# Optimization experiments

Measured on AMD Instinct MI355X. Metric: run time of the kernel, lower is better.

## Reference

```python
import jax, jax.numpy as jnp
import numpy as np

DIAG_PENALTY = 100.0

def setup_inputs() -> dict:
    key = jax.random.key(0)
    x = jax.random.normal(key, (8192, 768), dtype=jnp.float32)
    return {"x": x, "coef": 1.0, "tau": 1.0}

def _similarity(x):
    # sim[i, j] = -||x_i - x_j||^2, computed via GEMM expansion
    # ||a - b||^2 = ||a||^2 + ||b||^2 - 2 a.b  (avoids the (N,N,D) intermediate)
    sq = jnp.sum(x * x, axis=1)                      # [N]
    gram = x @ x.T                                   # [N, N]
    sim = 2.0 * gram - sq[:, None] - sq[None, :]     # = -||x_i - x_j||^2
    n = x.shape[0]
    sim = sim - DIAG_PENALTY * jnp.eye(n, dtype=x.dtype)
    return sim

def reference(x, coef, tau):
    sim = _similarity(x) * tau                       # [N, N]
    logp = jax.nn.log_softmax(sim, axis=-1)          # stable, single pass
    prob = jnp.exp(logp)
    entropy = -jnp.sum(prob * logp, axis=-1)         # [N]
    return coef * jnp.mean(entropy)
```

## Files before the change

### kernel.cpp

```cpp
#include <hip/hip_runtime.h>
#include <hip/hip_bf16.h>
#include <hip/hip_fp8.h>
#include <cstdint>
#include <cstddef>

#define GN 8192
#define GD 768
#define NB 64
#define NTILE 2080
#define KI 12

#define LOG2E 1.4426950408889634f
#define LN2 0.6931471805599453f

typedef __attribute__((ext_vector_type(4))) float f32x4;
typedef __attribute__((ext_vector_type(16))) float f32x16;
typedef __attribute__((ext_vector_type(4))) int i32x4;
typedef __attribute__((ext_vector_type(8))) int i32x8;

typedef __attribute__((address_space(1))) const unsigned int gu32;
typedef __attribute__((address_space(3))) unsigned int lu32;

#define SHUF8(L, H) __builtin_shufflevector(L, H, 0, 1, 2, 3, 4, 5, 6, 7)
#define Z16 {0.f, 0.f, 0.f, 0.f, 0.f, 0.f, 0.f, 0.f, 0.f, 0.f, 0.f, 0.f, 0.f, 0.f, 0.f, 0.f}
#define MXFMA(A, B, C) __builtin_amdgcn_mfma_scale_f32_32x32x64_f8f6f4( \
    A, B, C, 0, 0, 0, 0x7f7f7f7f, 0, 0x7f7f7f7f)

__device__ __forceinline__ void gl2lds16(const void* g, void* l) {
    __builtin_amdgcn_global_load_lds((gu32*)g, (lu32*)l, 16, 0, 0);
}

__device__ __forceinline__ float hexp2(float x) {
    return __builtin_amdgcn_exp2f(x);
}

template <int CTRL>
__device__ __forceinline__ float fdpp(float x) {
    return __int_as_float(__builtin_amdgcn_update_dpp(
        0, __float_as_int(x), CTRL, 0xF, 0xF, true));
}
__device__ __forceinline__ float qmax16(float v) {
    v = fmaxf(v, fdpp<0x128>(v));
    v = fmaxf(v, fdpp<0x124>(v));
    v = fmaxf(v, fdpp<0x122>(v));
    v = fmaxf(v, fdpp<0x121>(v));
    return v;
}
__device__ __forceinline__ float qsum16(float v) {
    v += fdpp<0x128>(v);
    v += fdpp<0x124>(v);
    v += fdpp<0x122>(v);
    v += fdpp<0x121>(v);
    return v;
}

__global__ __launch_bounds__(256) void prep_kernel(const float* __restrict__ x,
                                                   unsigned char* __restrict__ xq,
                                                   float* __restrict__ sq,
                                                   float* __restrict__ out) {
    if (blockIdx.x == 0 && threadIdx.x == 0) out[0] = 0.f;
    const int w = threadIdx.x >> 6, lane = threadIdx.x & 63;
    const int row = blockIdx.x * 4 + w;
    const float4* xr = (const float4*)(x + (size_t)row * GD);
    unsigned int* xqr = (unsigned int*)(xq + (size_t)row * GD);
    float s = 0.f;
#pragma unroll
    for (int i = 0; i < 3; ++i) {
        float4 v = xr[lane + 64 * i];
        unsigned int pk = __builtin_amdgcn_cvt_pk_fp8_f32(v.x, v.y, 0, false);
        pk = __builtin_amdgcn_cvt_pk_fp8_f32(v.z, v.w, pk, true);
        float d0 = __builtin_amdgcn_cvt_f32_fp8(pk, 0);
        float d1 = __builtin_amdgcn_cvt_f32_fp8(pk, 1);
        float d2 = __builtin_amdgcn_cvt_f32_fp8(pk, 2);
        float d3 = __builtin_amdgcn_cvt_f32_fp8(pk, 3);
        s += d0 * d0 + d1 * d1 + d2 * d2 + d3 * d3;
        xqr[lane + 64 * i] = pk;
    }
#pragma unroll
    for (int off = 1; off < 64; off <<= 1) s += __shfl_xor(s, off);
    if (lane == 0) sq[row] = s;
}

__global__ __launch_bounds__(256, 3) void sym_gemm_entropy(
    const unsigned char* __restrict__ xq, const float* __restrict__ sq,
    const float* __restrict__ taup, float* __restrict__ pm,
    float* __restrict__ ps, float* __restrict__ pt) {
    __shared__ __align__(16) char lds[16384];
    float (*tmrg)[4][3] = (float (*)[4][3])lds;

    const int tid = threadIdx.x;
    const int lane = tid & 63;
    const int w = tid >> 6;
    const int cl2 = lane & 31, hi = lane >> 5;

    const int b = blockIdx.x;
    int I = (int)((sqrtf(8.0f * (float)b + 1.0f) - 1.0f) * 0.5f);
    while ((I + 1) * (I + 2) / 2 <= b) ++I;
    while (I * (I + 1) / 2 > b) --I;
    const int J = b - I * (I + 1) / 2;
    const int row_base = I * 128;
    const int col_base = J * 128;
    const float taub = (*taup) * LOG2E;

    {
    }
    const int sS = tid & 127;
    const int ggS = tid >> 7;
    const int qloS = (sS >> 6) & 1, qhiS = (sS >> 5) & 1;
    const int r4S = (sS >> 4) & 1, r3S = (sS >> 3) & 1;
    const int rlowS = (sS & 7) ^ ((qhiS << 1) | r4S);
    const int rB = ggS * 32 + ((r4S << 4) | (r3S << 3) | rlowS);
    const int qB = (qhiS << 1) | qloS;
    const unsigned char* gB = xq + (size_t)(col_base + rB) * GD + qB * 16;

    const int r4L = (cl2 >> 4) & 1, r3L = (cl2 >> 3) & 1;
    const int bsl = (cl2 & 7) ^ ((hi << 1) | r4L);
    const int s0 = (hi << 5) | (r4L << 4) | (r3L << 3) | bsl;
    const int offB00 = 0 * 2048 + (s0 << 4), offB01 = offB00 + 1024;
    const int offB10 = 1 * 2048 + (s0 << 4), offB11 = offB10 + 1024;
    const int offB20 = 2 * 2048 + (s0 << 4), offB21 = offB20 + 1024;
    const int offB30 = 3 * 2048 + (s0 << 4), offB31 = offB30 + 1024;

    const unsigned char* gAr =
        xq + (size_t)(row_base + w * 32 + cl2) * GD + 32 * hi;

    f32x16 acc0 = Z16, acc1 = Z16, acc2 = Z16, acc3 = Z16;

    gl2lds16(gB, lds + tid * 16);
    gl2lds16(gB + (size_t)64 * GD, lds + 4096 + tid * 16);
    i32x4 aCL = *(const i32x4*)(gAr);
    i32x4 aCH = *(const i32x4*)(gAr + 16);
    i32x4 aNL = aCL, aNH = aCH;

#pragma unroll 2
    for (int kk = 0; kk < KI; ++kk) {
        __syncthreads();

        const char* Bb = lds + (kk & 1) * 8192;
        i32x4 b0L = *(const i32x4*)(Bb + offB00), b0H = *(const i32x4*)(Bb + offB01);
        i32x4 b1L = *(const i32x4*)(Bb + offB10), b1H = *(const i32x4*)(Bb + offB11);
        i32x4 b2L = *(const i32x4*)(Bb + offB20), b2H = *(const i32x4*)(Bb + offB21);
        i32x4 b3L = *(const i32x4*)(Bb + offB30), b3H = *(const i32x4*)(Bb + offB31);

        if (kk + 1 < KI) {
            char* Bn = lds + ((kk + 1) & 1) * 8192;
            const int ko = (kk + 1) * 64;
            gl2lds16(gB + ko, Bn + tid * 16);
            gl2lds16(gB + (size_t)64 * GD + ko, Bn + 4096 + tid * 16);
            aNL = *(const i32x4*)(gAr + ko);
            aNH = *(const i32x4*)(gAr + ko + 16);
        }

        i32x8 av = SHUF8(aCL, aCH);
        acc0 = MXFMA(av, SHUF8(b0L, b0H), acc0);
        acc1 = MXFMA(av, SHUF8(b1L, b1H), acc1);
        acc2 = MXFMA(av, SHUF8(b2L, b2H), acc2);
        acc3 = MXFMA(av, SHUF8(b3L, b3H), acc3);

        aCL = aNL;
        aCH = aNH;
    }

    f32x4 pa[4][4];
#define SPLIT16(TJ, A)                                          \
    pa[TJ][0] = __builtin_shufflevector(A, A, 0, 1, 2, 3);      \
    pa[TJ][1] = __builtin_shufflevector(A, A, 4, 5, 6, 7);      \
    pa[TJ][2] = __builtin_shufflevector(A, A, 8, 9, 10, 11);    \
    pa[TJ][3] = __builtin_shufflevector(A, A, 12, 13, 14, 15);
    SPLIT16(0, acc0)
    SPLIT16(1, acc1)
    SPLIT16(2, acc2)
    SPLIT16(3, acc3)
#undef SPLIT16

    const float t2 = 2.f * taub;
    const float pen = 100.f * taub;
    float ar[16];
#pragma unroll
    for (int q = 0; q < 4; ++q)
#pragma unroll
        for (int rg = 0; rg < 4; ++rg)
            ar[q * 4 + rg] = -taub * sq[row_base + w * 32 + rg + 8 * q + 4 * hi];
    float ac[4];
#pragma unroll
    for (int tj = 0; tj < 4; ++tj) ac[tj] = -taub * sq[col_base + tj * 32 + cl2];

    float* pmJ = pm + (size_t)J * GN;
    float* psJ = ps + (size_t)J * GN;
    float* ptJ = pt + (size_t)J * GN;

#pragma unroll
    for (int q = 0; q < 4; ++q)
#pragma unroll
        for (int rg = 0; rg < 4; ++rg) {
            const int rl = rg + 8 * q + 4 * hi;
            const int rglob = row_base + w * 32 + rl;
            float uu[4];
            float mloc = -1e30f;
            if (I == J) {
#pragma unroll
                for (int tj = 0; tj < 4; ++tj) {
                    float u = fmaf(t2, pa[tj][q][rg], ac[tj]);
                    if (rglob == col_base + tj * 32 + cl2) u -= pen;
                    uu[tj] = u;
                    mloc = fmaxf(mloc, u);
                }
            } else {
#pragma unroll
                for (int tj = 0; tj < 4; ++tj) {
                    float u = fmaf(t2, pa[tj][q][rg], ac[tj]);
                    uu[tj] = u;
                    mloc = fmaxf(mloc, u);
                }
            }
            mloc = fmaxf(mloc, __shfl_xor(mloc, 16));
            mloc = qmax16(mloc);
            float s = 0.f, t = 0.f;
#pragma unroll
            for (int tj = 0; tj < 4; ++tj) {
                float d = uu[tj] - mloc;
                float e = hexp2(d);
                s += e;
                t += e * d;
            }
            s += __shfl_xor(s, 16);
            t += __shfl_xor(t, 16);
            s = qsum16(s);
            t = qsum16(t);
            if (cl2 == 0) {
                pmJ[rglob] = mloc + ar[q * 4 + rg];
                psJ[rglob] = s;
                ptJ[rglob] = t;
            }
        }

    if (I != J) {
        __syncthreads();
#pragma unroll
        for (int tj = 0; tj < 4; ++tj) {
            float uu[16];
            float mloc = -1e30f;
#pragma unroll
            for (int q = 0; q < 4; ++q)
#pragma unroll
                for (int rg = 0; rg < 4; ++rg) {
                    float u = fmaf(t2, pa[tj][q][rg], ar[q * 4 + rg]);
                    uu[q * 4 + rg] = u;
                    mloc = fmaxf(mloc, u);
                }
            mloc = fmaxf(mloc, __shfl_xor(mloc, 32));
            float s = 0.f, t = 0.f;
#pragma unroll
            for (int k = 0; k < 16; ++k) {
                float d = uu[k] - mloc;
                float e = hexp2(d);
                s += e;
                t += e * d;
            }
            s += __shfl_xor(s, 32);
            t += __shfl_xor(t, 32);
            if (hi == 0) {
                int c = tj * 32 + cl2;
                tmrg[c][w][0] = mloc + ac[tj];
                tmrg[c][w][1] = s;
                tmrg[c][w][2] = t;
            }
        }
        __syncthreads();
        if (tid < 128) {
            float m = tmrg[tid][0][0], S = tmrg[tid][0][1], T = tmrg[tid][0][2];
#pragma unroll
            for (int ww = 1; ww < 4; ++ww) {
                float mc = tmrg[tid][ww][0], Sc = tmrg[tid][ww][1], Tc = tmrg[tid][ww][2];
                float mn = fmaxf(m, mc);
                float ea = hexp2(m - mn), eb = hexp2(mc - mn);
                T = (T + (m - mn) * S) * ea + (Tc + (mc - mn) * Sc) * eb;
                S = S * ea + Sc * eb;
                m = mn;
            }
            int c = col_base + tid;
            pm[(size_t)I * GN + c] = m;
            ps[(size_t)I * GN + c] = S;
            pt[(size_t)I * GN + c] = T;
        }
    }
}

__global__ __launch_bounds__(256) void combine(const float* __restrict__ pm,
                                               const float* __restrict__ ps,
                                               const float* __restrict__ pt,
                                               const float* __restrict__ coefp,
                                               float* __restrict__ out) {
    const int t = threadIdx.x;
    const int r = t & 63;
    const int chunk = t >> 6;
    const int row = blockIdx.x * 64 + r;
    float m = -1e30f, S = 0.f, T = 0.f;
#pragma unroll
    for (int i = 0; i < 16; ++i) {
        const int c = chunk * 16 + i;
        float mc = pm[(size_t)c * GN + row];
        float Sc = ps[(size_t)c * GN + row];
        float Tc = pt[(size_t)c * GN + row];
        float mn = fmaxf(m, mc);
        float ea = __builtin_amdgcn_exp2f(m - mn), eb = __builtin_amdgcn_exp2f(mc - mn);
        T = (T + (m - mn) * S) * ea + (Tc + (mc - mn) * Sc) * eb;
        S = S * ea + Sc * eb;
        m = mn;
    }
    __shared__ float lm[4][64], lS[4][64], lT[4][64];
    lm[chunk][r] = m;
    lS[chunk][r] = S;
    lT[chunk][r] = T;
    __syncthreads();
    if (t < 64) {
        float M = lm[0][r], Sa = lS[0][r], Ta = lT[0][r];
#pragma unroll
        for (int cc = 1; cc < 4; ++cc) {
            float mc = lm[cc][r], Sc = lS[cc][r], Tc = lT[cc][r];
            float mn = fmaxf(M, mc);
            float ea = __builtin_amdgcn_exp2f(M - mn), eb = __builtin_amdgcn_exp2f(mc - mn);
            Ta = (Ta + (M - mn) * Sa) * ea + (Tc + (mc - mn) * Sc) * eb;
            Sa = Sa * ea + Sc * eb;
            M = mn;
        }
        float ent2 = __log2f(Sa) - Ta / Sa;
#pragma unroll
        for (int off = 1; off < 64; off <<= 1) ent2 += __shfl_xor(ent2, off);
        if (t == 0) atomicAdd(out, ent2 * coefp[0] * (LN2 / (float)GN));
    }
}

extern "C" void kernel_launch(void* const* d_in, const int* in_sizes, int n_in,
                              void* d_out, int out_size, void* d_ws, size_t ws_size,
                              hipStream_t stream) {
    const float* x = (const float*)d_in[0];
    const float* coefp = (const float*)d_in[1];
    const float* taup = (const float*)d_in[2];
    float* out = (float*)d_out;

    char* ws = (char*)d_ws;
    unsigned char* xq = (unsigned char*)ws;
    float* sq = (float*)(ws + 6291456);
    float* pm = (float*)(ws + 6324224);
    float* ps = (float*)(ws + 6324224 + 2097152);
    float* pt = (float*)(ws + 6324224 + 2 * 2097152);

    prep_kernel<<<GN / 4, 256, 0, stream>>>(x, xq, sq, out);
    sym_gemm_entropy<<<NTILE, 256, 0, stream>>>(xq, sq, taup, pm, ps, pt);
    combine<<<GN / 64, 256, 0, stream>>>(pm, ps, pt, coefp, out);
}
```

Measured before the change: 149.1 us.

## Stage A tile through LDS with triple-buffered async prefetch pipeline

```diff
diff --git a/kernel.cpp b/kernel.cpp
--- a/kernel.cpp
+++ b/kernel.cpp
@@ -85,7 +85,7 @@
     const unsigned char* __restrict__ xq, const float* __restrict__ sq,
     const float* __restrict__ taup, float* __restrict__ pm,
     float* __restrict__ ps, float* __restrict__ pt) {
-    __shared__ __align__(16) char lds[16384];
+    __shared__ __align__(16) char lds[49152];
     float (*tmrg)[4][3] = (float (*)[4][3])lds;
 
     const int tid = threadIdx.x;
@@ -102,64 +102,64 @@
     const int col_base = J * 128;
     const float taub = (*taup) * LOG2E;
 
-    {
-    }
     const int sS = tid & 127;
-    const int ggS = tid >> 7;
+    const int g0S = tid >> 7;
     const int qloS = (sS >> 6) & 1, qhiS = (sS >> 5) & 1;
     const int r4S = (sS >> 4) & 1, r3S = (sS >> 3) & 1;
     const int rlowS = (sS & 7) ^ ((qhiS << 1) | r4S);
-    const int rB = ggS * 32 + ((r4S << 4) | (r3S << 3) | rlowS);
-    const int qB = (qhiS << 1) | qloS;
-    const unsigned char* gB = xq + (size_t)(col_base + rB) * GD + qB * 16;
+    const int rS = (r4S << 4) | (r3S << 3) | rlowS;
+    const int qS = (qhiS << 1) | qloS;
+    const unsigned char* gA = xq + (size_t)(row_base + g0S * 32 + rS) * GD + qS * 16;
+    const unsigned char* gB = xq + (size_t)(col_base + g0S * 32 + rS) * GD + qS * 16;
 
     const int r4L = (cl2 >> 4) & 1, r3L = (cl2 >> 3) & 1;
     const int bsl = (cl2 & 7) ^ ((hi << 1) | r4L);
     const int s0 = (hi << 5) | (r4L << 4) | (r3L << 3) | bsl;
-    const int offB00 = 0 * 2048 + (s0 << 4), offB01 = offB00 + 1024;
-    const int offB10 = 1 * 2048 + (s0 << 4), offB11 = offB10 + 1024;
-    const int offB20 = 2 * 2048 + (s0 << 4), offB21 = offB20 + 1024;
-    const int offB30 = 3 * 2048 + (s0 << 4), offB31 = offB30 + 1024;
-
-    const unsigned char* gAr =
-        xq + (size_t)(row_base + w * 32 + cl2) * GD + 32 * hi;
+    const int offA0 = w * 2048 + (s0 << 4), offA1 = offA0 + 1024;
+    const int offB00 = 8192 + 0 * 2048 + (s0 << 4), offB01 = offB00 + 1024;
+    const int offB10 = 8192 + 1 * 2048 + (s0 << 4), offB11 = offB10 + 1024;
+    const int offB20 = 8192 + 2 * 2048 + (s0 << 4), offB21 = offB20 + 1024;
+    const int offB30 = 8192 + 3 * 2048 + (s0 << 4), offB31 = offB30 + 1024;
 
     f32x16 acc0 = Z16, acc1 = Z16, acc2 = Z16, acc3 = Z16;
 
-    gl2lds16(gB, lds + tid * 16);
-    gl2lds16(gB + (size_t)64 * GD, lds + 4096 + tid * 16);
-    i32x4 aCL = *(const i32x4*)(gAr);
-    i32x4 aCH = *(const i32x4*)(gAr + 16);
-    i32x4 aNL = aCL, aNH = aCH;
-
-#pragma unroll 2
+#define STAGE(BUF, KO)                                                \
+    do {                                                              \
+        char* bn_ = lds + (BUF) * 16384;                              \
+        gl2lds16(gA + (KO), bn_ + tid * 16);                          \
+        gl2lds16(gA + (size_t)64 * GD + (KO), bn_ + 4096 + tid * 16); \
+        gl2lds16(gB + (KO), bn_ + 8192 + tid * 16);                   \
+        gl2lds16(gB + (size_t)64 * GD + (KO), bn_ + 12288 + tid * 16);\
+    } while (0)
+
+    STAGE(0, 0);
+    STAGE(1, 64);
+
+#pragma unroll
     for (int kk = 0; kk < KI; ++kk) {
-        __syncthreads();
-
-        const char* Bb = lds + (kk & 1) * 8192;
-        i32x4 b0L = *(const i32x4*)(Bb + offB00), b0H = *(const i32x4*)(Bb + offB01);
-        i32x4 b1L = *(const i32x4*)(Bb + offB10), b1H = *(const i32x4*)(Bb + offB11);
-        i32x4 b2L = *(const i32x4*)(Bb + offB20), b2H = *(const i32x4*)(Bb + offB21);
-        i32x4 b3L = *(const i32x4*)(Bb + offB30), b3H = *(const i32x4*)(Bb + offB31);
-
-        if (kk + 1 < KI) {
-            char* Bn = lds + ((kk + 1) & 1) * 8192;
-            const int ko = (kk + 1) * 64;
-            gl2lds16(gB + ko, Bn + tid * 16);
-            gl2lds16(gB + (size_t)64 * GD + ko, Bn + 4096 + tid * 16);
-            aNL = *(const i32x4*)(gAr + ko);
-            aNH = *(const i32x4*)(gAr + ko + 16);
-        }
-
-        i32x8 av = SHUF8(aCL, aCH);
+        if (kk < KI - 1)
+            asm volatile("s_waitcnt vmcnt(4)" ::: "memory");
+        else
+            asm volatile("s_waitcnt vmcnt(0)" ::: "memory");
+        __builtin_amdgcn_s_barrier();
+        __builtin_amdgcn_sched_barrier(0);
+
+        if (kk + 2 < KI) STAGE((kk + 2) % 3, (kk + 2) * 64);
+
+        const char* Ab = lds + (kk % 3) * 16384;
+        i32x4 aL = *(const i32x4*)(Ab + offA0), aH = *(const i32x4*)(Ab + offA1);
+        i32x4 b0L = *(const i32x4*)(Ab + offB00), b0H = *(const i32x4*)(Ab + offB01);
+        i32x4 b1L = *(const i32x4*)(Ab + offB10), b1H = *(const i32x4*)(Ab + offB11);
+        i32x4 b2L = *(const i32x4*)(Ab + offB20), b2H = *(const i32x4*)(Ab + offB21);
+        i32x4 b3L = *(const i32x4*)(Ab + offB30), b3H = *(const i32x4*)(Ab + offB31);
+
+        i32x8 av = SHUF8(aL, aH);
         acc0 = MXFMA(av, SHUF8(b0L, b0H), acc0);
         acc1 = MXFMA(av, SHUF8(b1L, b1H), acc1);
         acc2 = MXFMA(av, SHUF8(b2L, b2H), acc2);
         acc3 = MXFMA(av, SHUF8(b3L, b3H), acc3);
-
-        aCL = aNL;
-        aCH = aNH;
-    }
+    }
+#undef STAGE
 
     f32x4 pa[4][4];
 #define SPLIT16(TJ, A)                                          \
```

New measurement: 140.5 us. 1.06x faster.
